# Optimization experiments

Measured on AMD Instinct MI355X. Metric: run time of the kernel, lower is better.

Reference implementation:

```python
import jax, jax.numpy as jnp
import numpy as np

B, T, D, H = 2, 2048, 1024, 16
HD = D // H            # 64
FH = 2752              # SwiGLU hidden: round64(int(2*4*D/3))
BETA_INIT = 0.5


def rmsnorm(x, w, eps=1e-6):
    x32 = x.astype(jnp.float32)
    r = jax.lax.rsqrt(jnp.mean(x32 * x32, axis=-1, keepdims=True) + eps)
    return (x32 * r).astype(x.dtype) * w


def rope(x, cos, sin):
    # x: (B,H,T,HD); cos/sin: (T,HD//2)
    d2 = x.shape[-1] // 2
    x1, x2 = x[..., :d2], x[..., d2:]
    return jnp.concatenate([x1 * cos - x2 * sin, x2 * cos + x1 * sin], axis=-1)


def delta_res(x, h, gn_w, g_w, g_b, wv_w, eps_k=1e-6):
    # k-hat = normalize(h); k = k_hat / sqrt(d)
    h32 = h.astype(jnp.float32)
    nrm = jnp.sqrt(jnp.sum(h32 * h32, axis=-1, keepdims=True))
    k = (h32 / jnp.maximum(nrm, eps_k)).astype(x.dtype) * (1.0 / np.sqrt(D))
    c = rmsnorm(x, gn_w)
    logit = c @ g_w + g_b                                   # (B,T)
    beta = (2.0 * jax.nn.sigmoid(logit.astype(jnp.float32))).astype(x.dtype)[..., None]
    v = jax.nn.sigmoid(x @ wv_w)[..., None]                 # (B,T,1)
    kTx = jnp.sum(k * x, axis=-1, keepdims=True)
    return x + beta * (v - kTx) * k


def setup_inputs() -> dict:
    key = jax.random.key(0)
    ks = jax.random.split(key, 12)
    s = 0.02
    gb = np.float32(np.log(BETA_INIT / 2.0 / (1.0 - BETA_INIT / 2.0 + 1e-8)))
    return {
        "x": jax.random.normal(ks[0], (B, T, D), jnp.float32),
        "wq": jax.random.normal(ks[1], (D, D), jnp.float32) * s,
        "wk": jax.random.normal(ks[2], (D, D), jnp.float32) * s,
        "wv": jax.random.normal(ks[3], (D, D), jnp.float32) * s,
        "wo": jax.random.normal(ks[4], (D, D), jnp.float32) * s,
        "qn_w": jnp.ones((HD,), jnp.float32),
        "kn_w": jnp.ones((HD,), jnp.float32),
        "attn_norm_w": jnp.ones((D,), jnp.float32),
        "g1_norm_w": jnp.ones((D,), jnp.float32),
        "g1_w": jax.random.normal(ks[5], (D,), jnp.float32) * s,
        "g1_b": jnp.asarray(gb),
        "wv1": jax.random.normal(ks[6], (D,), jnp.float32) * s,
        "mlp_norm_w": jnp.ones((D,), jnp.float32),
        "w1": jax.random.normal(ks[7], (FH, D), jnp.float32) * s,
        "w2": jax.random.normal(ks[8], (D, FH), jnp.float32) * s,
        "w3": jax.random.normal(ks[9], (FH, D), jnp.float32) * s,
        "g2_norm_w": jnp.ones((D,), jnp.float32),
        "g2_w": jax.random.normal(ks[10], (D,), jnp.float32) * s,
        "g2_b": jnp.asarray(gb),
        "wv2": jax.random.normal(ks[11], (D,), jnp.float32) * s,
    }


def reference(x, wq, wk, wv, wo, qn_w, kn_w, attn_norm_w,
              g1_norm_w, g1_w, g1_b, wv1, mlp_norm_w, w1, w2, w3,
              g2_norm_w, g2_w, g2_b, wv2):
    # ---- attention sublayer (pre-norm) ----
    xc = rmsnorm(x, attn_norm_w)
    q = (xc @ wq.T).reshape(B, T, H, HD).swapaxes(1, 2)   # (B,H,T,HD)
    k = (xc @ wk.T).reshape(B, T, H, HD).swapaxes(1, 2)
    v = (xc @ wv.T).reshape(B, T, H, HD).swapaxes(1, 2)
    q = rmsnorm(q, qn_w)
    k = rmsnorm(k, kn_w)
    inv_freq = 1.0 / (10000.0 ** (jnp.arange(0, HD, 2, dtype=jnp.float32) / HD))
    freqs = jnp.arange(T, dtype=jnp.float32)[:, None] * inv_freq[None, :]  # (T,HD/2)
    cos, sin = jnp.cos(freqs), jnp.sin(freqs)
    q = rope(q, cos, sin)
    k = rope(k, cos, sin)
    scale = 1.0 / np.sqrt(HD)
    scores = jnp.einsum('bhqd,bhkd->bhqk', q, k) * scale
    causal = jnp.where(jnp.arange(T)[:, None] >= jnp.arange(T)[None, :], 0.0, -jnp.inf).astype(scores.dtype)
    attn = jax.nn.softmax(scores + causal, axis=-1)
    out = jnp.einsum('bhqk,bhkd->bhqd', attn, v)
    h_attn = out.swapaxes(1, 2).reshape(B, T, D) @ wo.T
    x = delta_res(x, h_attn, g1_norm_w, g1_w, g1_b, wv1)
    # ---- MLP sublayer (pre-norm SwiGLU) ----
    xm = rmsnorm(x, mlp_norm_w)
    h_mlp = (jax.nn.silu(xm @ w1.T) * (xm @ w3.T)) @ w2.T
    x = delta_res(x, h_mlp, g2_norm_w, g2_w, g2_b, wv2)
    return x
```

## Files before the change

### kernel.cpp

```cpp
#include <hip/hip_runtime.h>
#include <hip/hip_bf16.h>
#include <math.h>

using bf16 = __hip_bfloat16;
typedef __bf16 bf16x8 __attribute__((ext_vector_type(8)));
typedef float f32x4 __attribute__((ext_vector_type(4)));

static constexpr int B_ = 2, T_ = 2048, D_ = 1024, H_ = 16, HD_ = 64, FH_ = 2752;
static constexpr int BT = B_ * T_;

struct __align__(8)  bh4 { bf16 h[4]; };
struct __align__(16) bh8 { bf16 h[8]; };

#define DEV static __device__ __forceinline__

DEV float b2f(bf16 v) { return __bfloat162float(v); }
DEV bf16  f2b(float v) { return __float2bfloat16(v); }
DEV __bf16 f2bb(float f) { __hip_bfloat16 h = __float2bfloat16(f); return *reinterpret_cast<__bf16*>(&h); }
DEV float sigmoidf_(float x) { return 1.0f / (1.0f + __expf(-x)); }

DEV void load4f(const bf16* p, float* v) {
    bh4 t = *reinterpret_cast<const bh4*>(p);
#pragma unroll
    for (int i = 0; i < 4; ++i) v[i] = b2f(t.h[i]);
}
DEV void load4f(const float* p, float* v) {
    float4 t = *reinterpret_cast<const float4*>(p);
    v[0] = t.x; v[1] = t.y; v[2] = t.z; v[3] = t.w;
}
DEV void store4(float* p, const float* v) {
    float4 t; t.x = v[0]; t.y = v[1]; t.z = v[2]; t.w = v[3];
    *reinterpret_cast<float4*>(p) = t;
}
DEV float waveReduceSum(float v) {
#pragma unroll
    for (int m = 32; m; m >>= 1) v += __shfl_xor(v, m);
    return v;
}

DEV void gl_lds16(const bf16* g, bf16* lds_base) {
    __builtin_amdgcn_global_load_lds(
        (const __attribute__((address_space(1))) void*)g,
        (__attribute__((address_space(3))) void*)lds_base, 16, 0, 0);
}

__global__ __launch_bounds__(256) void k_rope_tables(float* __restrict__ cost, float* __restrict__ sint) {
    int idx = blockIdx.x * 256 + threadIdx.x;
    if (idx >= T_ * 32) return;
    int t = idx >> 5, j = idx & 31;
    float inv = powf(10000.0f, -(float)j * (1.0f / 32.0f));
    float f = (float)t * inv;
    cost[idx] = cosf(f);
    sint[idx] = sinf(f);
}

__global__ __launch_bounds__(256) void k_f2b(const float* __restrict__ in, bf16* __restrict__ out, int n8) {
    int i = blockIdx.x * 256 + threadIdx.x;
    if (i >= n8) return;
    const float4* p = reinterpret_cast<const float4*>(in + (size_t)i * 8);
    float4 a = p[0], b = p[1];
    bh8 o;
    o.h[0] = f2b(a.x); o.h[1] = f2b(a.y); o.h[2] = f2b(a.z); o.h[3] = f2b(a.w);
    o.h[4] = f2b(b.x); o.h[5] = f2b(b.y); o.h[6] = f2b(b.z); o.h[7] = f2b(b.w);
    *reinterpret_cast<bh8*>(out + (size_t)i * 8) = o;
}

__global__ __launch_bounds__(256) void k_f2b_pair(const float* __restrict__ w1, const float* __restrict__ w3,
                                                  bf16* __restrict__ outp, int n8tot) {
    int i = blockIdx.x * 256 + threadIdx.x;
    if (i >= n8tot) return;
    int r = i >> 7, c8 = i & 127;
    int sel = (r >> 4) & 1;
    int j = ((r >> 5) << 4) | (r & 15);
    const float* src = (sel ? w3 : w1) + (size_t)j * D_ + c8 * 8;
    float4 a = reinterpret_cast<const float4*>(src)[0];
    float4 b = reinterpret_cast<const float4*>(src)[1];
    bh8 o;
    o.h[0] = f2b(a.x); o.h[1] = f2b(a.y); o.h[2] = f2b(a.z); o.h[3] = f2b(a.w);
    o.h[4] = f2b(b.x); o.h[5] = f2b(b.y); o.h[6] = f2b(b.z); o.h[7] = f2b(b.w);
    *reinterpret_cast<bh8*>(outp + (size_t)r * D_ + c8 * 8) = o;
}

__global__ __launch_bounds__(256) void k_rmsnorm(const float* __restrict__ x, const float* __restrict__ w,
                                                 bf16* __restrict__ out) {
    int row = blockIdx.x, tid = threadIdx.x;
    const float* xr = x + (size_t)row * D_;
    int base = tid * 4;
    float v[4];
    load4f(xr + base, v);
    float ss = v[0]*v[0] + v[1]*v[1] + v[2]*v[2] + v[3]*v[3];
    ss = waveReduceSum(ss);
    __shared__ float red[4];
    if ((tid & 63) == 0) red[tid >> 6] = ss;
    __syncthreads();
    ss = red[0] + red[1] + red[2] + red[3];
    float r = rsqrtf(ss * (1.0f / D_) + 1e-6f);
    float wv[4];
    load4f(w + base, wv);
    bh4 o;
#pragma unroll
    for (int i = 0; i < 4; ++i) o.h[i] = f2b(v[i] * r * wv[i]);
    *reinterpret_cast<bh4*>(out + (size_t)row * D_ + base) = o;
}

template <int EPI>
__global__ __launch_bounds__(512) void k_gemm256(const bf16* __restrict__ A, const bf16* __restrict__ W,
                                                 bf16* __restrict__ C, int M, int N, int K) {
    __shared__ bf16 sA[2][256 * 32];
    __shared__ bf16 sB[2][128 * 32];
    int tid = threadIdx.x, lane = tid & 63, wid = tid >> 6;
    int nwg = gridDim.x;
    int swz = (blockIdx.x & 7) * (nwg >> 3) + (blockIdx.x >> 3);
    int gxm = M >> 8;
    int m0 = (swz % gxm) * 256, n0 = (swz / gxm) * 128;
    int wr = wid >> 1, wc = wid & 1;
    int l16 = lane & 15, lg = lane >> 4;
    int srow = lane >> 2;
    int scol = ((lane & 3) ^ ((lane >> 3) & 3)) * 8;
    int rchunk = (lg ^ ((l16 >> 1) & 3)) * 8;

    f32x4 acc[4][4] = {};

#define STAGE(buf, k0)                                                                   \
    {                                                                                    \
        _Pragma("unroll")                                                                \
        for (int c = 0; c < 2; ++c) {                                                    \
            int r0 = wid * 32 + c * 16;                                                  \
            gl_lds16(&A[(size_t)(m0 + r0 + srow) * K + (k0) + scol], &sA[buf][r0 * 32]); \
        }                                                                                \
        {                                                                                \
            int r0 = wid * 16;                                                           \
            gl_lds16(&W[(size_t)(n0 + r0 + srow) * K + (k0) + scol], &sB[buf][r0 * 32]); \
        }                                                                                \
    }

    STAGE(0, 0);
    __syncthreads();
    int nk = K >> 5;
    int cur = 0;
    for (int t = 0; t < nk; ++t) {
        if (t + 1 < nk) STAGE(cur ^ 1, (t + 1) * 32);
        bf16x8 af[4], bfr[4];
#pragma unroll
        for (int m = 0; m < 4; ++m)
            af[m] = *reinterpret_cast<const bf16x8*>(&sA[cur][(wr * 64 + m * 16 + l16) * 32 + rchunk]);
#pragma unroll
        for (int n = 0; n < 4; ++n)
            bfr[n] = *reinterpret_cast<const bf16x8*>(&sB[cur][(wc * 64 + n * 16 + l16) * 32 + rchunk]);
#pragma unroll
        for (int m = 0; m < 4; ++m)
#pragma unroll
            for (int n = 0; n < 4; ++n)
                acc[m][n] = __builtin_amdgcn_mfma_f32_16x16x32_bf16(af[m], bfr[n], acc[m][n], 0, 0, 0);
        __syncthreads();
        cur ^= 1;
    }
#undef STAGE

    int rbase = m0 + wr * 64;
    if (EPI == 1) {
        int Ng = N >> 1;
        int gbase = (n0 >> 1) + wc * 32;
#pragma unroll
        for (int m = 0; m < 4; ++m) {
#pragma unroll
            for (int n2 = 0; n2 < 2; ++n2) {
                int gcol = gbase + n2 * 16 + l16;
#pragma unroll
                for (int r = 0; r < 4; ++r) {
                    int row = rbase + m * 16 + lg * 4 + r;
                    float a1 = acc[m][n2 * 2][r];
                    float a3 = acc[m][n2 * 2 + 1][r];
                    C[(size_t)row * Ng + gcol] = f2b(a1 * sigmoidf_(a1) * a3);
                }
            }
        }
    } else {
        int cbase = n0 + wc * 64;
#pragma unroll
        for (int m = 0; m < 4; ++m) {
#pragma unroll
            for (int n = 0; n < 4; ++n) {
                int col = cbase + n * 16 + l16;
#pragma unroll
                for (int r = 0; r < 4; ++r) {
                    int row = rbase + m * 16 + lg * 4 + r;
                    C[(size_t)row * N + col] = f2b(acc[m][n][r]);
                }
            }
        }
    }
}

__global__ __launch_bounds__(256) void k_gemm64(const bf16* __restrict__ A, const bf16* __restrict__ W,
                                                bf16* __restrict__ C, int M, int N, int K) {
    __shared__ bf16 sA[2][128 * 32];
    __shared__ bf16 sB[2][64 * 32];
    int tid = threadIdx.x, lane = tid & 63, wid = tid >> 6;
    int nwg = gridDim.x;
    int swz = (blockIdx.x & 7) * (nwg >> 3) + (blockIdx.x >> 3);
    int gxm = M >> 7;
    int m0 = (swz % gxm) * 128, n0 = (swz / gxm) * 64;
    int wr = wid;
    int l16 = lane & 15, lg = lane >> 4;
    int srow = lane >> 2;
    int scol = ((lane & 3) ^ ((lane >> 3) & 3)) * 8;
    int rchunk = (lg ^ ((l16 >> 1) & 3)) * 8;

    f32x4 acc[2][4] = {};

#define STAGE(buf, k0)                                                                   \
    {                                                                                    \
        _Pragma("unroll")                                                                \
        for (int c = 0; c < 2; ++c) {                                                    \
            int r0 = wid * 32 + c * 16;                                                  \
            gl_lds16(&A[(size_t)(m0 + r0 + srow) * K + (k0) + scol], &sA[buf][r0 * 32]); \
        }                                                                                \
        {                                                                                \
            int r0 = wid * 16;                                                           \
            gl_lds16(&W[(size_t)(n0 + r0 + srow) * K + (k0) + scol], &sB[buf][r0 * 32]); \
        }                                                                                \
    }

    STAGE(0, 0);
    __syncthreads();
    int nk = K >> 5;
    int cur = 0;
    for (int t = 0; t < nk; ++t) {
        if (t + 1 < nk) STAGE(cur ^ 1, (t + 1) * 32);
        bf16x8 af[2], bfr[4];
#pragma unroll
        for (int m = 0; m < 2; ++m)
            af[m] = *reinterpret_cast<const bf16x8*>(&sA[cur][(wr * 32 + m * 16 + l16) * 32 + rchunk]);
#pragma unroll
        for (int n = 0; n < 4; ++n)
            bfr[n] = *reinterpret_cast<const bf16x8*>(&sB[cur][(n * 16 + l16) * 32 + rchunk]);
#pragma unroll
        for (int m = 0; m < 2; ++m)
#pragma unroll
            for (int n = 0; n < 4; ++n)
                acc[m][n] = __builtin_amdgcn_mfma_f32_16x16x32_bf16(af[m], bfr[n], acc[m][n], 0, 0, 0);
        __syncthreads();
        cur ^= 1;
    }
#undef STAGE

    int rbase = m0 + wr * 32;
#pragma unroll
    for (int m = 0; m < 2; ++m) {
#pragma unroll
        for (int n = 0; n < 4; ++n) {
            int col = n0 + n * 16 + l16;
#pragma unroll
            for (int r = 0; r < 4; ++r) {
                int row = rbase + m * 16 + lg * 4 + r;
                C[(size_t)row * N + col] = f2b(acc[m][n][r]);
            }
        }
    }
}

__global__ __launch_bounds__(256) void k_qk_norm_rope(const bf16* __restrict__ qin, const float* __restrict__ wn,
                                                      const float* __restrict__ cost, const float* __restrict__ sint,
                                                      bf16* __restrict__ qout, float scale, int ld, int off) {
    int tid = threadIdx.x;
    int g = blockIdx.x * 4 + (tid >> 6);
    int d = tid & 63;
    int h = g % H_, t = (g / H_) % T_, b = g / (H_ * T_);
    float v = b2f(qin[(size_t)(b * T_ + t) * ld + off + h * HD_ + d]);
    float ss = waveReduceSum(v * v);
    float r = rsqrtf(ss * (1.0f / HD_) + 1e-6f);
    float xn = v * r * wn[d];
    float p = __shfl_xor(xn, 32);
    float c = cost[t * 32 + (d & 31)], s = sint[t * 32 + (d & 31)];
    float o = (d < 32) ? (xn * c - p * s) : (xn * c + p * s);
    qout[((size_t)(b * H_ + h) * T_ + t) * HD_ + d] = f2b(o * scale);
}

__global__ __launch_bounds__(256) void k_v_transpose(const bf16* __restrict__ vin, bf16* __restrict__ vt,
                                                     int ld, int off) {
    __shared__ bf16 tile[64][72];
    int tid = threadIdx.x;
    int bh = blockIdx.y;
    int t0 = blockIdx.x * 64;
    int b = bh >> 4, h = bh & 15;
#pragma unroll
    for (int i = 0; i < 16; ++i) {
        int lin = i * 256 + tid;
        int tl = lin >> 6, d = lin & 63;
        tile[tl][d] = vin[(size_t)(b * T_ + t0 + tl) * ld + off + h * HD_ + d];
    }
    __syncthreads();
#pragma unroll
    for (int i = 0; i < 16; ++i) {
        int lin = i * 256 + tid;
        int d = lin >> 6, tl = lin & 63;
        vt[((size_t)bh * HD_ + d) * T_ + t0 + tl] = tile[tl][d];
    }
}

template <bool MASKED>
DEV void fa3_tile(const bf16* __restrict__ kl, const bf16* __restrict__ vl,
                  int l16, int lg, int qloc,
                  const bf16x8 qf0, const bf16x8 qf1,
                  f32x4* acc, float& m_r, float& l_r) {
    f32x4 s[8];
#pragma unroll
    for (int n = 0; n < 8; ++n) {
        int kv = n * 16 + l16;
        bf16x8 kf0 = *reinterpret_cast<const bf16x8*>(&kl[kv * 64 + (((lg ^ kv) & 7) << 3)]);
        bf16x8 kf1 = *reinterpret_cast<const bf16x8*>(&kl[kv * 64 + ((((4 + lg) ^ kv) & 7) << 3)]);
        f32x4 t = {};
        t = __builtin_amdgcn_mfma_f32_16x16x32_bf16(kf0, qf0, t, 0, 0, 0);
        t = __builtin_amdgcn_mfma_f32_16x16x32_bf16(kf1, qf1, t, 0, 0, 0);
        s[n] = t;
    }
    if (MASKED) {
#pragma unroll
        for (int n = 0; n < 8; ++n)
#pragma unroll
            for (int r = 0; r < 4; ++r)
                if (n * 16 + lg * 4 + r > qloc) s[n][r] = -INFINITY;
    }
    float mx = -INFINITY;
#pragma unroll
    for (int n = 0; n < 8; ++n)
#pragma unroll
        for (int r = 0; r < 4; ++r) mx = fmaxf(mx, s[n][r]);
    mx = fmaxf(mx, __shfl_xor(mx, 16));
    mx = fmaxf(mx, __shfl_xor(mx, 32));
    float mnew = fmaxf(m_r, mx);
    float corr = __expf(m_r - mnew);
    m_r = mnew;
    float ps = 0.0f;
#pragma unroll
    for (int n = 0; n < 8; ++n)
#pragma unroll
        for (int r = 0; r < 4; ++r) {
            float e = __expf(s[n][r] - mnew);
            s[n][r] = e;
            ps += e;
        }
    l_r = l_r * corr + ps;
#pragma unroll
    for (int np = 0; np < 4; ++np) acc[np] = acc[np] * corr;

    bf16x8 pb[4];
#pragma unroll
    for (int n2 = 0; n2 < 4; ++n2)
#pragma unroll
        for (int j = 0; j < 8; ++j)
            pb[n2][j] = f2bb(s[2 * n2 + (j >> 2)][j & 3]);

    int d15 = l16;
    int eoff = (lg & 1) * 4;
#pragma unroll
    for (int n2 = 0; n2 < 4; ++n2) {
        int c0 = (n2 * 4 + (lg >> 1));
        int c1 = c0 + 2;
#pragma unroll
        for (int np = 0; np < 4; ++np) {
            int d = np * 16 + l16;
            union { bf16x8 v; bh4 q[2]; } u;
            u.q[0] = *reinterpret_cast<const bh4*>(&vl[d * 128 + ((c0 ^ d15) << 3) + eoff]);
            u.q[1] = *reinterpret_cast<const bh4*>(&vl[d * 128 + ((c1 ^ d15) << 3) + eoff]);
            acc[np] = __builtin_amdgcn_mfma_f32_16x16x32_bf16(u.v, pb[n2], acc[np], 0, 0, 0);
        }
    }
}

__global__ __launch_bounds__(256) void k_flash(const bf16* __restrict__ Q, const bf16* __restrict__ Kk,
                                               const bf16* __restrict__ Vt, bf16* __restrict__ Out) {
    __shared__ bf16 kl[128 * 64];
    __shared__ bf16 vl[64 * 128];
    int tid = threadIdx.x, lane = tid & 63, w = tid >> 6;
    int l16 = lane & 15, lg = lane >> 4;
    int L = blockIdx.x;
    int xcd = L & 7, m = L >> 3;
    int bh = xcd * 4 + (m & 3);
    int qi = (T_ / 128 - 1) - (m >> 2);
    int q0 = qi * 128;
    int b = bh >> 4, h = bh & 15;
    const bf16* qb = Q + (size_t)bh * T_ * HD_;
    const bf16* kb = Kk + (size_t)bh * T_ * HD_;
    const bf16* vb = Vt + (size_t)bh * HD_ * T_;

    bf16x8 qfr[2][2];
#pragma unroll
    for (int f = 0; f < 2; ++f) {
        int qrow = q0 + w * 32 + f * 16 + l16;
        const bf16* qp = qb + (size_t)qrow * HD_ + lg * 8;
        qfr[f][0] = *reinterpret_cast<const bf16x8*>(qp);
        qfr[f][1] = *reinterpret_cast<const bf16x8*>(qp + 32);
    }
    f32x4 acc[2][4] = {};
    float m_r[2] = {-INFINITY, -INFINITY};
    float l_r[2] = {0.0f, 0.0f};

    for (int kv0 = 0; kv0 <= q0; kv0 += 128) {
        __syncthreads();
#pragma unroll
        for (int i = 0; i < 4; ++i) {
            int idx = i * 256 + tid;
            int kv = idx >> 3, c = idx & 7;
            *reinterpret_cast<bh8*>(&kl[kv * 64 + (((c ^ kv) & 7) << 3)]) =
                *reinterpret_cast<const bh8*>(&kb[(size_t)(kv0 + kv) * HD_ + c * 8]);
        }
#pragma unroll
        for (int i = 0; i < 4; ++i) {
            int idx = i * 256 + tid;
            int d = idx >> 4, c = idx & 15;
            *reinterpret_cast<bh8*>(&vl[d * 128 + (((c ^ d) & 15) << 3)]) =
                *reinterpret_cast<const bh8*>(&vb[(size_t)d * T_ + kv0 + c * 8]);
        }
        __syncthreads();
        if (kv0 == q0) {
#pragma unroll
            for (int f = 0; f < 2; ++f)
                fa3_tile<true>(kl, vl, l16, lg, w * 32 + f * 16 + l16,
                               qfr[f][0], qfr[f][1], acc[f], m_r[f], l_r[f]);
        } else {
#pragma unroll
            for (int f = 0; f < 2; ++f)
                fa3_tile<false>(kl, vl, l16, lg, 0,
                                qfr[f][0], qfr[f][1], acc[f], m_r[f], l_r[f]);
        }
    }
#pragma unroll
    for (int f = 0; f < 2; ++f) {
        float lt = l_r[f];
        lt += __shfl_xor(lt, 16);
        lt += __shfl_xor(lt, 32);
        float inv = 1.0f / lt;
        int qrow = q0 + w * 32 + f * 16 + l16;
#pragma unroll
        for (int np = 0; np < 4; ++np) {
            bh4 o;
#pragma unroll
            for (int r = 0; r < 4; ++r) o.h[r] = f2b(acc[f][np][r] * inv);
            *reinterpret_cast<bh4*>(&Out[(size_t)(b * T_ + qrow) * D_ + h * HD_ + np * 16 + lg * 4]) = o;
        }
    }
}

template <int WRITE_XM>
__global__ __launch_bounds__(256) void k_delta_res(const float* __restrict__ x, const bf16* __restrict__ h,
                                                   const float* __restrict__ gn_w, const float* __restrict__ g_w,
                                                   const float* __restrict__ g_b, const float* __restrict__ wv_w,
                                                   float* __restrict__ out,
                                                   bf16* __restrict__ xm_out, const float* __restrict__ mlp_w) {
    int row = blockIdx.x, tid = threadIdx.x;
    int base = tid * 4;
    float xv[4], hv[4], gnv[4], gwv[4], wvv[4];
    load4f(x + (size_t)row * D_ + base, xv);
    load4f(h + (size_t)row * D_ + base, hv);
    load4f(gn_w + base, gnv);
    load4f(g_w + base, gwv);
    load4f(wv_w + base, wvv);
    float s_h2 = 0, s_x2 = 0, s_xg = 0, s_xv = 0, s_hx = 0;
#pragma unroll
    for (int i = 0; i < 4; ++i) {
        s_h2 += hv[i] * hv[i];
        s_x2 += xv[i] * xv[i];
        s_xg += xv[i] * gnv[i] * gwv[i];
        s_xv += xv[i] * wvv[i];
        s_hx += hv[i] * xv[i];
    }
    s_h2 = waveReduceSum(s_h2); s_x2 = waveReduceSum(s_x2); s_xg = waveReduceSum(s_xg);
    s_xv = waveReduceSum(s_xv); s_hx = waveReduceSum(s_hx);
    __shared__ float red[4][5];
    int wid = tid >> 6;
    if ((tid & 63) == 0) {
        red[wid][0] = s_h2; red[wid][1] = s_x2; red[wid][2] = s_xg;
        red[wid][3] = s_xv; red[wid][4] = s_hx;
    }
    __syncthreads();
    s_h2 = red[0][0] + red[1][0] + red[2][0] + red[3][0];
    s_x2 = red[0][1] + red[1][1] + red[2][1] + red[3][1];
    s_xg = red[0][2] + red[1][2] + red[2][2] + red[3][2];
    s_xv = red[0][3] + red[1][3] + red[2][3] + red[3][3];
    s_hx = red[0][4] + red[1][4] + red[2][4] + red[3][4];

    float r = rsqrtf(s_x2 * (1.0f / D_) + 1e-6f);
    float logit = r * s_xg + g_b[0];
    float beta = 2.0f * sigmoidf_(logit);
    float vsig = sigmoidf_(s_xv);
    float nrm = sqrtf(s_h2);
    float ks = (1.0f / 32.0f) / fmaxf(nrm, 1e-6f);
    float coef = beta * (vsig - ks * s_hx) * ks;
    float o[4];
#pragma unroll
    for (int i = 0; i < 4; ++i) o[i] = xv[i] + coef * hv[i];
    store4(out + (size_t)row * D_ + base, o);

    if (WRITE_XM) {
        float s2 = o[0]*o[0] + o[1]*o[1] + o[2]*o[2] + o[3]*o[3];
        s2 = waveReduceSum(s2);
        __shared__ float red2[4];
        __syncthreads();
        if ((tid & 63) == 0) red2[wid] = s2;
        __syncthreads();
        s2 = red2[0] + red2[1] + red2[2] + red2[3];
        float rr = rsqrtf(s2 * (1.0f / D_) + 1e-6f);
        float mw[4];
        load4f(mlp_w + base, mw);
        bh4 ob;
#pragma unroll
        for (int i = 0; i < 4; ++i) ob.h[i] = f2b(o[i] * rr * mw[i]);
        *reinterpret_cast<bh4*>(xm_out + (size_t)row * D_ + base) = ob;
    }
}

extern "C" void kernel_launch(void* const* d_in, const int* in_sizes, int n_in,
                              void* d_out, int out_size, void* d_ws, size_t ws_size,
                              hipStream_t stream) {
    const float* x       = (const float*)d_in[0];
    const float* wq      = (const float*)d_in[1];
    const float* wk      = (const float*)d_in[2];
    const float* wv      = (const float*)d_in[3];
    const float* wo      = (const float*)d_in[4];
    const float* qn_w    = (const float*)d_in[5];
    const float* kn_w    = (const float*)d_in[6];
    const float* attn_nw = (const float*)d_in[7];
    const float* g1_nw   = (const float*)d_in[8];
    const float* g1_w    = (const float*)d_in[9];
    const float* g1_b    = (const float*)d_in[10];
    const float* wv1     = (const float*)d_in[11];
    const float* mlp_nw  = (const float*)d_in[12];
    const float* w1      = (const float*)d_in[13];
    const float* w2      = (const float*)d_in[14];
    const float* w3      = (const float*)d_in[15];
    const float* g2_nw   = (const float*)d_in[16];
    const float* g2_w    = (const float*)d_in[17];
    const float* g2_b    = (const float*)d_in[18];
    const float* wv2     = (const float*)d_in[19];
    float* out = (float*)d_out;

    char* ws = (char*)d_ws;
    const size_t KB = 1024;
    const size_t MB = 1024 * 1024;
    float* cost = (float*)(ws);
    float* sint = (float*)(ws + 256 * KB);
    bf16* XC = (bf16*)(ws + 512 * KB);
    bf16* Bb = (bf16*)(ws + 512 * KB + 8  * MB);
    bf16* Cb = (bf16*)(ws + 512 * KB + 16 * MB);
    bf16* Db = (bf16*)(ws + 512 * KB + 24 * MB);
    bf16* Eb = (bf16*)(ws + 512 * KB + 32 * MB);
    bf16* Fb = (bf16*)(ws + 512 * KB + 40 * MB);
    bf16* Gb = (bf16*)(ws + 512 * KB + 48 * MB);
    float* x1 = (float*)(ws + 512 * KB + 56 * MB);

    bf16* wqkv = Eb;
    bf16* qkv  = Bb;
    bf16* wbo  = XC;
    bf16* attn_out = Bb;
    bf16* wpair = Bb;
    bf16* w2b  = Db;
    bf16* g    = Eb;
    bf16* hmlp = XC;

    const int nDD = D_ * D_ / 8, nFD = FH_ * D_ / 8;
    dim3 blk(256);

    k_rope_tables<<<dim3((T_ * 32) / 256), blk, 0, stream>>>(cost, sint);

    k_rmsnorm<<<dim3(BT), blk, 0, stream>>>(x, attn_nw, XC);
    k_f2b<<<dim3((nDD + 255) / 256), blk, 0, stream>>>(wq, wqkv, nDD);
    k_f2b<<<dim3((nDD + 255) / 256), blk, 0, stream>>>(wk, wqkv + (size_t)D_ * D_, nDD);
    k_f2b<<<dim3((nDD + 255) / 256), blk, 0, stream>>>(wv, wqkv + (size_t)2 * D_ * D_, nDD);

    k_gemm256<0><<<dim3(16 * 24), dim3(512), 0, stream>>>(XC, wqkv, qkv, BT, 3 * D_, D_);

    k_qk_norm_rope<<<dim3(BT * H_ / 4), blk, 0, stream>>>(qkv, qn_w, cost, sint, Eb, 0.125f, 3 * D_, 0);
    k_qk_norm_rope<<<dim3(BT * H_ / 4), blk, 0, stream>>>(qkv, kn_w, cost, sint, Fb, 1.0f, 3 * D_, D_);
    k_v_transpose<<<dim3(T_ / 64, B_ * H_), blk, 0, stream>>>(qkv, Gb, 3 * D_, 2 * D_);

    k_f2b<<<dim3((nDD + 255) / 256), blk, 0, stream>>>(wo, wbo, nDD);
    k_flash<<<dim3((T_ / 128) * B_ * H_), blk, 0, stream>>>(Eb, Fb, Gb, attn_out);

    k_gemm64<<<dim3(32 * 16), blk, 0, stream>>>(attn_out, wbo, Cb, BT, D_, D_);

    k_delta_res<1><<<dim3(BT), blk, 0, stream>>>(x, Cb, g1_nw, g1_w, g1_b, wv1, x1, XC, mlp_nw);

    k_f2b_pair<<<dim3((2 * nFD + 255) / 256), blk, 0, stream>>>(w1, w3, wpair, 2 * nFD);
    k_f2b<<<dim3((nFD + 255) / 256), blk, 0, stream>>>(w2, w2b, nFD);

    k_gemm256<1><<<dim3(16 * 43), dim3(512), 0, stream>>>(XC, wpair, g, BT, 2 * FH_, D_);

    k_gemm64<<<dim3(32 * 16), blk, 0, stream>>>(g, w2b, hmlp, BT, D_, FH_);

    k_delta_res<0><<<dim3(BT), blk, 0, stream>>>(x1, hmlp, g2_nw, g2_w, g2_b, wv2, out, nullptr, nullptr);
}
```

Baseline: 290.7 us.

## Issue GEMM tile loads two stages ahead with explicit vmcnt waits; drop block swizzle

Both GEMM kernels now prefetch the first two K-tiles up front and refill each LDS buffer two iterations ahead. Completion is tracked with explicit s_waitcnt vmcnt counts and raw s_barrier calls instead of __syncthreads, so global-to-LDS loads overlap more of the MFMA work. The grid also becomes a plain 2D launch, dropping the XCD-aware block swizzle. The hardcoded vmcnt(3) assumes exactly three outstanding loads per stage, and removing the swizzle can hurt L2 locality across chiplets.

```diff
diff --git a/kernel.cpp b/kernel.cpp
--- a/kernel.cpp
+++ b/kernel.cpp
@@ -109,10 +109,7 @@
     __shared__ bf16 sA[2][256 * 32];
     __shared__ bf16 sB[2][128 * 32];
     int tid = threadIdx.x, lane = tid & 63, wid = tid >> 6;
-    int nwg = gridDim.x;
-    int swz = (blockIdx.x & 7) * (nwg >> 3) + (blockIdx.x >> 3);
-    int gxm = M >> 8;
-    int m0 = (swz % gxm) * 256, n0 = (swz / gxm) * 128;
+    int m0 = blockIdx.x * 256, n0 = blockIdx.y * 128;
     int wr = wid >> 1, wc = wid & 1;
     int l16 = lane & 15, lg = lane >> 4;
     int srow = lane >> 2;
@@ -134,12 +131,15 @@
         }                                                                                \
     }
 
+    int nk = K >> 5;
     STAGE(0, 0);
-    __syncthreads();
-    int nk = K >> 5;
-    int cur = 0;
+    if (nk > 1) STAGE(1, 32);
     for (int t = 0; t < nk; ++t) {
-        if (t + 1 < nk) STAGE(cur ^ 1, (t + 1) * 32);
+        if (t + 1 < nk) { asm volatile("s_waitcnt vmcnt(3)" ::: "memory"); }
+        else            { asm volatile("s_waitcnt vmcnt(0)" ::: "memory"); }
+        __builtin_amdgcn_s_barrier();
+        __builtin_amdgcn_sched_barrier(0);
+        int cur = t & 1;
         bf16x8 af[4], bfr[4];
 #pragma unroll
         for (int m = 0; m < 4; ++m)
@@ -152,8 +152,9 @@
 #pragma unroll
             for (int n = 0; n < 4; ++n)
                 acc[m][n] = __builtin_amdgcn_mfma_f32_16x16x32_bf16(af[m], bfr[n], acc[m][n], 0, 0, 0);
-        __syncthreads();
-        cur ^= 1;
+        __builtin_amdgcn_sched_barrier(0);
+        __builtin_amdgcn_s_barrier();
+        if (t + 2 < nk) STAGE(cur, (t + 2) * 32);
     }
 #undef STAGE
 
@@ -197,10 +198,7 @@
     __shared__ bf16 sA[2][128 * 32];
     __shared__ bf16 sB[2][64 * 32];
     int tid = threadIdx.x, lane = tid & 63, wid = tid >> 6;
-    int nwg = gridDim.x;
-    int swz = (blockIdx.x & 7) * (nwg >> 3) + (blockIdx.x >> 3);
-    int gxm = M >> 7;
-    int m0 = (swz % gxm) * 128, n0 = (swz / gxm) * 64;
+    int m0 = blockIdx.x * 128, n0 = blockIdx.y * 64;
     int wr = wid;
     int l16 = lane & 15, lg = lane >> 4;
     int srow = lane >> 2;
@@ -222,12 +220,15 @@
         }                                                                                \
     }
 
+    int nk = K >> 5;
     STAGE(0, 0);
-    __syncthreads();
-    int nk = K >> 5;
-    int cur = 0;
+    if (nk > 1) STAGE(1, 32);
     for (int t = 0; t < nk; ++t) {
-        if (t + 1 < nk) STAGE(cur ^ 1, (t + 1) * 32);
+        if (t + 1 < nk) { asm volatile("s_waitcnt vmcnt(3)" ::: "memory"); }
+        else            { asm volatile("s_waitcnt vmcnt(0)" ::: "memory"); }
+        __builtin_amdgcn_s_barrier();
+        __builtin_amdgcn_sched_barrier(0);
+        int cur = t & 1;
         bf16x8 af[2], bfr[4];
 #pragma unroll
         for (int m = 0; m < 2; ++m)
@@ -240,8 +241,9 @@
 #pragma unroll
             for (int n = 0; n < 4; ++n)
                 acc[m][n] = __builtin_amdgcn_mfma_f32_16x16x32_bf16(af[m], bfr[n], acc[m][n], 0, 0, 0);
-        __syncthreads();
-        cur ^= 1;
+        __builtin_amdgcn_sched_barrier(0);
+        __builtin_amdgcn_s_barrier();
+        if (t + 2 < nk) STAGE(cur, (t + 2) * 32);
     }
 #undef STAGE
 
@@ -569,7 +571,7 @@
     k_f2b<<<dim3((nDD + 255) / 256), blk, 0, stream>>>(wk, wqkv + (size_t)D_ * D_, nDD);
     k_f2b<<<dim3((nDD + 255) / 256), blk, 0, stream>>>(wv, wqkv + (size_t)2 * D_ * D_, nDD);
 
-    k_gemm256<0><<<dim3(16 * 24), dim3(512), 0, stream>>>(XC, wqkv, qkv, BT, 3 * D_, D_);
+    k_gemm256<0><<<dim3(16, 24), dim3(512), 0, stream>>>(XC, wqkv, qkv, BT, 3 * D_, D_);
 
     k_qk_norm_rope<<<dim3(BT * H_ / 4), blk, 0, stream>>>(qkv, qn_w, cost, sint, Eb, 0.125f, 3 * D_, 0);
     k_qk_norm_rope<<<dim3(BT * H_ / 4), blk, 0, stream>>>(qkv, kn_w, cost, sint, Fb, 1.0f, 3 * D_, D_);
@@ -578,16 +580,16 @@
     k_f2b<<<dim3((nDD + 255) / 256), blk, 0, stream>>>(wo, wbo, nDD);
     k_flash<<<dim3((T_ / 128) * B_ * H_), blk, 0, stream>>>(Eb, Fb, Gb, attn_out);
 
-    k_gemm64<<<dim3(32 * 16), blk, 0, stream>>>(attn_out, wbo, Cb, BT, D_, D_);
+    k_gemm64<<<dim3(32, 16), blk, 0, stream>>>(attn_out, wbo, Cb, BT, D_, D_);
 
     k_delta_res<1><<<dim3(BT), blk, 0, stream>>>(x, Cb, g1_nw, g1_w, g1_b, wv1, x1, XC, mlp_nw);
 
     k_f2b_pair<<<dim3((2 * nFD + 255) / 256), blk, 0, stream>>>(w1, w3, wpair, 2 * nFD);
     k_f2b<<<dim3((nFD + 255) / 256), blk, 0, stream>>>(w2, w2b, nFD);
 
-    k_gemm256<1><<<dim3(16 * 43), dim3(512), 0, stream>>>(XC, wpair, g, BT, 2 * FH_, D_);
-
-    k_gemm64<<<dim3(32 * 16), blk, 0, stream>>>(g, w2b, hmlp, BT, D_, FH_);
+    k_gemm256<1><<<dim3(16, 43), dim3(512), 0, stream>>>(XC, wpair, g, BT, 2 * FH_, D_);
+
+    k_gemm64<<<dim3(32, 16), blk, 0, stream>>>(g, w2b, hmlp, BT, D_, FH_);
 
     k_delta_res<0><<<dim3(BT), blk, 0, stream>>>(x1, hmlp, g2_nw, g2_w, g2_b, wv2, out, nullptr, nullptr);
 }
```

New measurement: 282.9 us. 1.03x faster.
